# Kernel optimization log

Hardware: AMD Instinct MI355X
Metric: run time of the kernel (lower is better)

## Reference

```python
import jax, jax.numpy as jnp
import numpy as np

B, N, D = 2, 2048, 1024
H, ENC = 16, 8
HD = D // H
EPS = 1e-5


def _apply_rope(x, cos, sin):
    # x: [B,N,H,HD], cos/sin: [N,HD//2]
    c = cos[None, :, None, :]
    s = sin[None, :, None, :]
    x_re = x[..., 0::2]
    x_im = x[..., 1::2]
    out = jnp.stack([x_re * c - x_im * s, x_re * s + x_im * c], axis=-1)
    return out.reshape(x.shape)


def _rmsnorm(x):
    return x * jax.lax.rsqrt(jnp.mean(x * x, axis=-1, keepdims=True) + EPS)


def setup_inputs() -> dict:
    key = jax.random.key(0)
    ks = jax.random.split(key, 8)
    pos = jnp.arange(N, dtype=jnp.float32)[:, None]
    inv_freq = 1.0 / (10000.0 ** (jnp.arange(0, HD, 2, dtype=jnp.float32) / HD))  # [HD//2]
    ang = pos * inv_freq[None, :]
    std = 0.02
    return {
        "x": jax.random.normal(ks[0], (B, N, D), dtype=jnp.float32),
        "rope_cos": jnp.cos(ang),
        "rope_sin": jnp.sin(ang),
        "Wq": std * jax.random.normal(ks[1], (D, D), dtype=jnp.float32),
        "Wk": std * jax.random.normal(ks[2], (D, D), dtype=jnp.float32),
        "Wv": std * jax.random.normal(ks[3], (D, D), dtype=jnp.float32),
        "Wo_enc": std * jax.random.normal(ks[4], (H * HD, D), dtype=jnp.float32),
        "Wo_dec": std * jax.random.normal(ks[5], ((H - ENC) * HD, D), dtype=jnp.float32),
        "heads": H,
        "encoder_heads": ENC,
    }


def reference(x, rope_cos, rope_sin, Wq, Wk, Wv, Wo_enc, Wo_dec, heads, encoder_heads):
    b, n, d = x.shape
    hd = d // heads
    scale = hd ** (-0.5)
    q = (x @ Wq).reshape(b, n, heads, hd)
    k = (x @ Wk).reshape(b, n, heads, hd)
    v = (x @ Wv).reshape(b, n, heads, hd)
    q = _rmsnorm(_apply_rope(q, rope_cos, rope_sin))
    k = _rmsnorm(_apply_rope(k, rope_cos, rope_sin))
    # scores: [B,H,N,N]
    scores = jnp.einsum("bihd,bjhd->bhij", q, k) * scale
    causal = jnp.tril(jnp.ones((n, n), dtype=bool))  # [N,N]
    is_enc = (jnp.arange(heads) < encoder_heads)[:, None, None]  # [H,1,1]
    allow = jnp.logical_or(is_enc, causal[None, :, :])  # [H,N,N]
    scores = jnp.where(allow[None], scores, -jnp.inf)
    att = jax.nn.softmax(scores, axis=-1)
    out = jnp.einsum("bhij,bjhd->bihd", att, v)  # [B,N,H,HD]
    enc_out = out.reshape(b, n, heads * hd) @ Wo_enc
    dec_out = out[:, :, encoder_heads:, :].reshape(b, n, (heads - encoder_heads) * hd) @ Wo_dec
    return (enc_out, dec_out)
```

## Files before the change

### kernel.cpp

```cpp
#include <hip/hip_runtime.h>
#include <hip/hip_bf16.h>
#include <math.h>

#define B_    2
#define N_    2048
#define D_    1024
#define H_    16
#define ENC_  8
#define HD_   64
#define EPS_  1e-5f
#define M_    (B_ * N_)

typedef __bf16 bf16x8 __attribute__((ext_vector_type(8)));
typedef __bf16 bf16x2 __attribute__((ext_vector_type(2)));
typedef float  f32x4  __attribute__((ext_vector_type(4)));

#define MB(x) ((size_t)(x) * 1024 * 1024)

#define KSC_  0.18033688011112042f

#if __has_builtin(__builtin_amdgcn_exp2f)
#define EXP2F(x) __builtin_amdgcn_exp2f(x)
#else
#define EXP2F(x) exp2f(x)
#endif

__device__ __forceinline__ void gld16(const __bf16* g, __bf16* l) {
    __builtin_amdgcn_global_load_lds(
        (const __attribute__((address_space(1))) void*)g,
        (__attribute__((address_space(3))) void*)l,
        16, 0, 0);
}

template <typename OutT>
__device__ __forceinline__ void gemm_core(
    const __bf16* __restrict__ A, const __bf16* __restrict__ Bt,
    OutT* __restrict__ C, int K, int lda, int aoff, int ldc,
    int bm, int bn, __bf16* As, __bf16* Bs)
{
    const int tid  = threadIdx.x;
    const int w    = tid >> 6;
    const int lane = tid & 63;
    const int lrow = lane & 15;
    const int quad = lane >> 4;
    const int wr   = w >> 1;
    const int wc   = w & 1;

    const int sr = lane >> 2;
    const int sc = (lane & 3) * 8;
    const __bf16* Ag0 = A  + (size_t)(bm +      w * 16 + sr) * lda + aoff + sc;
    const __bf16* Ag1 = A  + (size_t)(bm + 64 + w * 16 + sr) * lda + aoff + sc;
    const __bf16* Bg0 = Bt + (size_t)(bn +      w * 16 + sr) * K + sc;
    const __bf16* Bg1 = Bt + (size_t)(bn + 64 + w * 16 + sr) * K + sc;
    __bf16* Al0 = &As[w * 512];
    __bf16* Al1 = &As[2048 + w * 512];
    __bf16* Bl0 = &Bs[w * 512];
    __bf16* Bl1 = &Bs[2048 + w * 512];

    f32x4 acc[4][4];
    #pragma unroll
    for (int i = 0; i < 4; ++i)
        #pragma unroll
        for (int j = 0; j < 4; ++j) acc[i][j] = (f32x4){0.f, 0.f, 0.f, 0.f};

    for (int k0 = 0; k0 < K; k0 += 32) {
        gld16(Ag0 + k0, Al0);
        gld16(Ag1 + k0, Al1);
        gld16(Bg0 + k0, Bl0);
        gld16(Bg1 + k0, Bl1);
        __syncthreads();

        bf16x8 af[4], bf[4];
        #pragma unroll
        for (int rt = 0; rt < 4; ++rt)
            af[rt] = *(const bf16x8*)&As[(wr * 64 + rt * 16 + lrow) * 32 + quad * 8];
        #pragma unroll
        for (int ct = 0; ct < 4; ++ct)
            bf[ct] = *(const bf16x8*)&Bs[(wc * 64 + ct * 16 + lrow) * 32 + quad * 8];

        #pragma unroll
        for (int rt = 0; rt < 4; ++rt)
            #pragma unroll
            for (int ct = 0; ct < 4; ++ct)
                acc[rt][ct] = __builtin_amdgcn_mfma_f32_16x16x32_bf16(
                    af[rt], bf[ct], acc[rt][ct], 0, 0, 0);
        __syncthreads();
    }

    #pragma unroll
    for (int rt = 0; rt < 4; ++rt)
        #pragma unroll
        for (int ct = 0; ct < 4; ++ct)
            #pragma unroll
            for (int r = 0; r < 4; ++r) {
                const int row = bm + wr * 64 + rt * 16 + quad * 4 + r;
                const int col = bn + wc * 64 + ct * 16 + lrow;
                C[(size_t)row * ldc + col] = (OutT)acc[rt][ct][r];
            }
}

__global__ __launch_bounds__(256) void gemm_qkv(
    const __bf16* __restrict__ A, const __bf16* __restrict__ Bt,
    __bf16* __restrict__ C)
{
    __shared__ __bf16 As[128 * 32];
    __shared__ __bf16 Bs[128 * 32];
    gemm_core<__bf16>(A, Bt, C, D_, D_, 0, 3072,
                      blockIdx.y * 128, blockIdx.x * 128, As, Bs);
}

__global__ __launch_bounds__(256) void gemm_out(
    const __bf16* __restrict__ A, const __bf16* __restrict__ Woe,
    const __bf16* __restrict__ Wod, float* __restrict__ Cenc,
    float* __restrict__ Cdec)
{
    __shared__ __bf16 As[128 * 32];
    __shared__ __bf16 Bs[128 * 32];
    const int bx = blockIdx.x;
    if (bx < 8) {
        gemm_core<float>(A, Woe, Cenc, 1024, D_, 0, D_,
                         blockIdx.y * 128, bx * 128, As, Bs);
    } else {
        gemm_core<float>(A, Wod, Cdec, 512, D_, 512, D_,
                         blockIdx.y * 128, (bx - 8) * 128, As, Bs);
    }
}

__global__ __launch_bounds__(256) void f32_to_bf16(
    const float* __restrict__ src, __bf16* __restrict__ dst)
{
    const size_t i = ((size_t)blockIdx.x * 256 + threadIdx.x) * 8;
    float4 a = *(const float4*)&src[i];
    float4 b = *(const float4*)&src[i + 4];
    bf16x8 o = {(__bf16)a.x, (__bf16)a.y, (__bf16)a.z, (__bf16)a.w,
                (__bf16)b.x, (__bf16)b.y, (__bf16)b.z, (__bf16)b.w};
    *(bf16x8*)&dst[i] = o;
}

struct WtArgs {
    const float* W[5];
    __bf16*      Wt[5];
    int          K[5];
    int          nyb[5];
};

__global__ __launch_bounds__(256) void wt_conv_all(WtArgs a)
{
    const int z = blockIdx.z;
    if (blockIdx.y >= a.nyb[z]) return;
    const float* W  = a.W[z];
    __bf16*      Wt = a.Wt[z];
    const int    K  = a.K[z];

    __shared__ __bf16 t[64][72];
    const int kb = blockIdx.y * 64;
    const int nb = blockIdx.x * 64;
    {
        const int kl = threadIdx.x >> 2;
        const int c0 = (threadIdx.x & 3) * 16;
        const float* src = W + (size_t)(kb + kl) * D_ + nb + c0;
        #pragma unroll
        for (int u = 0; u < 4; ++u) {
            float4 f = *(const float4*)&src[u * 4];
            t[c0 + u * 4 + 0][kl] = (__bf16)f.x;
            t[c0 + u * 4 + 1][kl] = (__bf16)f.y;
            t[c0 + u * 4 + 2][kl] = (__bf16)f.z;
            t[c0 + u * 4 + 3][kl] = (__bf16)f.w;
        }
    }
    __syncthreads();
    {
        const int nl  = threadIdx.x >> 2;
        const int k0c = (threadIdx.x & 3) * 16;
        __bf16* dst = Wt + (size_t)(nb + nl) * K + kb + k0c;
        *(bf16x8*)&dst[0] = *(const bf16x8*)&t[nl][k0c];
        *(bf16x8*)&dst[8] = *(const bf16x8*)&t[nl][k0c + 8];
    }
}

__global__ __launch_bounds__(256) void rope_vconv(
    const __bf16* __restrict__ qkv,
    const float* __restrict__ cs, const float* __restrict__ sn,
    __bf16* __restrict__ qbf, __bf16* __restrict__ kbf,
    __bf16* __restrict__ vt)
{
    if (blockIdx.x < 16384) {
        const int row  = blockIdx.x * 4 + (threadIdx.x >> 6);
        const int lane = threadIdx.x & 63;
        const int n    = (row >> 4) & (N_ - 1);
        const int b    = row >> 15;
        const int h    = row & 15;
        const int p    = lane >> 1;

        const float c = cs[n * (HD_ / 2) + p];
        const float s = sn[n * (HD_ / 2) + p];
        const size_t ibase = (size_t)(b * N_ + n) * 3072 + h * HD_ + lane;
        const size_t obase = ((size_t)(b * H_ + h) * N_ + n) * HD_ + lane;
        const bool odd = (lane & 1);

        {
            float val = (float)qkv[ibase];
            float partner = __shfl_xor(val, 1, 64);
            float r = odd ? fmaf(partner, s, val * c)
                          : (val * c - partner * s);
            float ss = r * r;
            #pragma unroll
            for (int off = 1; off < 64; off <<= 1) ss += __shfl_xor(ss, off, 64);
            qbf[obase] = (__bf16)(r * rsqrtf(ss * (1.0f / 64.0f) + EPS_) * KSC_);
        }
        {
            float val = (float)qkv[ibase + 1024];
            float partner = __shfl_xor(val, 1, 64);
            float r = odd ? fmaf(partner, s, val * c)
                          : (val * c - partner * s);
            float ss = r * r;
            #pragma unroll
            for (int off = 1; off < 64; off <<= 1) ss += __shfl_xor(ss, off, 64);
            kbf[obase] = (__bf16)(r * rsqrtf(ss * (1.0f / 64.0f) + EPS_));
        }
    } else {
        __shared__ __bf16 tile[64][72];
        const int bx = blockIdx.x - 16384;
        const int bh = bx >> 5;
        const int b  = bh >> 4, h = bh & 15;
        const int n0 = (bx & 31) * 64;
        {
            const int nl = threadIdx.x >> 2;
            const int d0 = (threadIdx.x & 3) * 16;
            const __bf16* src =
                qkv + (size_t)(b * N_ + n0 + nl) * 3072 + 2048 + h * HD_ + d0;
            bf16x8 v0 = *(const bf16x8*)&src[0];
            bf16x8 v1 = *(const bf16x8*)&src[8];
            #pragma unroll
            for (int e = 0; e < 8; ++e) {
                tile[d0 + e][nl]     = v0[e];
                tile[d0 + 8 + e][nl] = v1[e];
            }
        }
        __syncthreads();
        {
            const int dl = threadIdx.x >> 2;
            const int nc = (threadIdx.x & 3) * 16;
            __bf16* dst = vt + ((size_t)(bh * HD_ + dl)) * N_ + n0 + nc;
            bf16x8 o0, o1;
            #pragma unroll
            for (int e = 0; e < 8; ++e) {
                const int p0 = nc + e;
                const int p1 = nc + 8 + e;
                o0[e] = tile[dl][(p0 & ~31) + (((p0 >> 2) & 1) << 4)
                                 + (((p0 >> 3) & 3) << 2) + (p0 & 3)];
                o1[e] = tile[dl][(p1 & ~31) + (((p1 >> 2) & 1) << 4)
                                 + (((p1 >> 3) & 3) << 2) + (p1 & 3)];
            }
            *(bf16x8*)&dst[0] = o0;
            *(bf16x8*)&dst[8] = o1;
        }
    }
}

template <int NG, bool DEC>
__device__ __forceinline__ void attn_core(
    const __bf16* __restrict__ qbase, const __bf16* __restrict__ kbase,
    const __bf16* __restrict__ vbase, __bf16* __restrict__ o,
    int b, int h, int qb, int ntiles,
    __bf16 (*Ks)[4096], __bf16 (*Vs)[4096])
{
    const int tid  = threadIdx.x;
    const int w    = tid >> 6;
    const int lane = tid & 63;
    const int lrow = lane & 15;
    const int quad = lane >> 4;

    const __bf16* kg0 = kbase + (size_t)lane * HD_ + w * 8;
    const __bf16* kg1 = kbase + (size_t)lane * HD_ + (w + 4) * 8;
    const __bf16* vg  = vbase + (size_t)lane * N_;

    int i0g[NG];
    #pragma unroll
    for (int g = 0; g < NG; ++g) i0g[g] = qb * (NG * 64) + g * 64 + w * 16;

    bf16x8 qf[NG][2];
    #pragma unroll
    for (int g = 0; g < NG; ++g)
        #pragma unroll
        for (int kc = 0; kc < 2; ++kc)
            qf[g][kc] = *(const bf16x8*)
                &qbase[(size_t)(i0g[g] + lrow) * HD_ + kc * 32 + quad * 8];

    const f32x4 zero = {0.f, 0.f, 0.f, 0.f};
    f32x4 oacc[NG][4];
    float lsum[NG];
    #pragma unroll
    for (int g = 0; g < NG; ++g) {
        lsum[g] = 0.f;
        #pragma unroll
        for (int c = 0; c < 4; ++c) oacc[g][c] = zero;
    }

    auto stage = [&](int t, int bb) {
        const int j0 = t << 6;
        gld16(kg0 + (size_t)j0 * HD_, &Ks[bb][(w)     * 512]);
        gld16(kg1 + (size_t)j0 * HD_, &Ks[bb][(w + 4) * 512]);
        gld16(vg + j0 + w * 8,        &Vs[bb][(w)     * 512]);
        gld16(vg + j0 + (w + 4) * 8,  &Vs[bb][(w + 4) * 512]);
    };

    stage(0, 0);
    for (int t = 0; t < ntiles; ++t) {
        const int bb = t & 1;
        __syncthreads();
        if (t + 1 < ntiles) stage(t + 1, bb ^ 1);

        #pragma unroll
        for (int s = 0; s < 2; ++s) {
            const int jp = (t << 6) + s * 32;

            bf16x8 kf0 = *(const bf16x8*)&Ks[bb][((quad)     * 64 + s * 32 + lrow) * 8];
            bf16x8 kf1 = *(const bf16x8*)&Ks[bb][((4 + quad) * 64 + s * 32 + lrow) * 8];
            bf16x8 kf2 = *(const bf16x8*)&Ks[bb][((quad)     * 64 + s * 32 + 16 + lrow) * 8];
            bf16x8 kf3 = *(const bf16x8*)&Ks[bb][((4 + quad) * 64 + s * 32 + 16 + lrow) * 8];

            f32x4 s0[NG], s1[NG];
            #pragma unroll
            for (int g = 0; g < NG; ++g) { s0[g] = zero; s1[g] = zero; }
            #pragma unroll
            for (int g = 0; g < NG; ++g)
                s0[g] = __builtin_amdgcn_mfma_f32_16x16x32_bf16(kf0, qf[g][0], s0[g], 0, 0, 0);
            #pragma unroll
            for (int g = 0; g < NG; ++g)
                s0[g] = __builtin_amdgcn_mfma_f32_16x16x32_bf16(kf1, qf[g][1], s0[g], 0, 0, 0);
            #pragma unroll
            for (int g = 0; g < NG; ++g)
                s1[g] = __builtin_amdgcn_mfma_f32_16x16x32_bf16(kf2, qf[g][0], s1[g], 0, 0, 0);
            #pragma unroll
            for (int g = 0; g < NG; ++g)
                s1[g] = __builtin_amdgcn_mfma_f32_16x16x32_bf16(kf3, qf[g][1], s1[g], 0, 0, 0);

            bf16x8 pf[NG];
            #pragma unroll
            for (int g = 0; g < NG; ++g) {
                float pA[4], pB[4];
                if (DEC && (jp + 31 > i0g[g])) {
                    const int i = i0g[g] + lrow;
                    #pragma unroll
                    for (int r = 0; r < 4; ++r) {
                        const int k0 = jp + quad * 4 + r;
                        pA[r] = (k0      <= i) ? EXP2F(s0[g][r]) : 0.f;
                        pB[r] = (k0 + 16 <= i) ? EXP2F(s1[g][r]) : 0.f;
                    }
                } else {
                    #pragma unroll
                    for (int r = 0; r < 4; ++r) {
                        pA[r] = EXP2F(s0[g][r]);
                        pB[r] = EXP2F(s1[g][r]);
                    }
                }
                lsum[g] += (pA[0] + pA[1]) + (pA[2] + pA[3])
                         + (pB[0] + pB[1]) + (pB[2] + pB[3]);
                pf[g] = (bf16x8){(__bf16)pA[0], (__bf16)pA[1],
                                 (__bf16)pA[2], (__bf16)pA[3],
                                 (__bf16)pB[0], (__bf16)pB[1],
                                 (__bf16)pB[2], (__bf16)pB[3]};
            }

            bf16x8 vf0 = *(const bf16x8*)&Vs[bb][((s * 4 + quad) * 64 +  0 + lrow) * 8];
            bf16x8 vf1 = *(const bf16x8*)&Vs[bb][((s * 4 + quad) * 64 + 16 + lrow) * 8];
            bf16x8 vf2 = *(const bf16x8*)&Vs[bb][((s * 4 + quad) * 64 + 32 + lrow) * 8];
            bf16x8 vf3 = *(const bf16x8*)&Vs[bb][((s * 4 + quad) * 64 + 48 + lrow) * 8];

            #pragma unroll
            for (int g = 0; g < NG; ++g) {
                oacc[g][0] = __builtin_amdgcn_mfma_f32_16x16x32_bf16(pf[g], vf0, oacc[g][0], 0, 0, 0);
                oacc[g][1] = __builtin_amdgcn_mfma_f32_16x16x32_bf16(pf[g], vf1, oacc[g][1], 0, 0, 0);
                oacc[g][2] = __builtin_amdgcn_mfma_f32_16x16x32_bf16(pf[g], vf2, oacc[g][2], 0, 0, 0);
                oacc[g][3] = __builtin_amdgcn_mfma_f32_16x16x32_bf16(pf[g], vf3, oacc[g][3], 0, 0, 0);
            }
        }
    }

    float lrec[NG][4];
    #pragma unroll
    for (int g = 0; g < NG; ++g) {
        float s = lsum[g];
        s += __shfl_xor(s, 16, 64);
        s += __shfl_xor(s, 32, 64);
        s = 1.0f / s;
        #pragma unroll
        for (int r = 0; r < 4; ++r)
            lrec[g][r] = __shfl(s, quad * 4 + r, 64);
    }

    #pragma unroll
    for (int g = 0; g < NG; ++g)
        #pragma unroll
        for (int c = 0; c < 4; ++c)
            #pragma unroll
            for (int r = 0; r < 4; ++r) {
                const int i = i0g[g] + quad * 4 + r;
                o[(size_t)(b * N_ + i) * D_ + h * HD_ + c * 16 + lrow] =
                    (__bf16)(oacc[g][c][r] * lrec[g][r]);
            }
}

__global__ __launch_bounds__(256) void attn_mfma(
    const __bf16* __restrict__ qbf, const __bf16* __restrict__ kbf,
    const __bf16* __restrict__ vtbf, __bf16* __restrict__ o)
{
    __shared__ __bf16 Ks[2][4096];
    __shared__ __bf16 Vs[2][4096];

    if (blockIdx.x < 256) {
        const int e  = blockIdx.x & 15;
        const int bh = (e >> 3) * 16 + (e & 7);
        const int qb = blockIdx.x >> 4;
        attn_core<2, false>(
            qbf  + (size_t)bh * N_ * HD_, kbf + (size_t)bh * N_ * HD_,
            vtbf + (size_t)bh * HD_ * N_, o,
            bh >> 4, bh & 15, qb, N_ >> 6, Ks, Vs);
    } else {
        const int idx = blockIdx.x - 256;
        const int d   = idx & 15;
        const int bh  = (d >> 3) * 16 + 8 + (d & 7);
        const int qb  = 31 - (idx >> 4);
        attn_core<1, true>(
            qbf  + (size_t)bh * N_ * HD_, kbf + (size_t)bh * N_ * HD_,
            vtbf + (size_t)bh * HD_ * N_, o,
            bh >> 4, bh & 15, qb, qb + 1, Ks, Vs);
    }
}

extern "C" void kernel_launch(void* const* d_in, const int* in_sizes, int n_in,
                              void* d_out, int out_size, void* d_ws, size_t ws_size,
                              hipStream_t stream)
{
    const float* x   = (const float*)d_in[0];
    const float* cs  = (const float*)d_in[1];
    const float* sn  = (const float*)d_in[2];
    const float* Wq  = (const float*)d_in[3];
    const float* Wk  = (const float*)d_in[4];
    const float* Wv  = (const float*)d_in[5];
    const float* Woe = (const float*)d_in[6];
    const float* Wod = (const float*)d_in[7];

    float* enc_out = (float*)d_out;
    float* dec_out = enc_out + (size_t)M_ * D_;

    char* ws = (char*)d_ws;
    __bf16* xbf    = (__bf16*)(ws);
    __bf16* wqkv_t = (__bf16*)(ws + MB(8));
    __bf16* woe_t  = (__bf16*)(ws + MB(14));
    __bf16* wod_t  = (__bf16*)(ws + MB(16));
    __bf16* qkv    = (__bf16*)(ws + MB(17));
    __bf16* qbf    = (__bf16*)(ws + MB(41));
    __bf16* kbf    = (__bf16*)(ws + MB(49));
    __bf16* vtbf   = xbf;
    __bf16* obuf   = qkv;

    f32_to_bf16<<<(M_ * D_) / (256 * 8), 256, 0, stream>>>(x, xbf);

    WtArgs wa;
    wa.W[0] = Wq;  wa.Wt[0] = wqkv_t;                 wa.K[0] = 1024; wa.nyb[0] = 16;
    wa.W[1] = Wk;  wa.Wt[1] = wqkv_t + 1024 * 1024;   wa.K[1] = 1024; wa.nyb[1] = 16;
    wa.W[2] = Wv;  wa.Wt[2] = wqkv_t + 2048 * 1024;   wa.K[2] = 1024; wa.nyb[2] = 16;
    wa.W[3] = Woe; wa.Wt[3] = woe_t;                  wa.K[3] = 1024; wa.nyb[3] = 16;
    wa.W[4] = Wod; wa.Wt[4] = wod_t;                  wa.K[4] = 512;  wa.nyb[4] = 8;
    wt_conv_all<<<dim3(16, 16, 5), 256, 0, stream>>>(wa);

    gemm_qkv<<<dim3(3072 / 128, M_ / 128), 256, 0, stream>>>(xbf, wqkv_t, qkv);

    rope_vconv<<<16384 + 1024, 256, 0, stream>>>(qkv, cs, sn, qbf, kbf, vtbf);

    attn_mfma<<<dim3(768), 256, 0, stream>>>(qbf, kbf, vtbf, obuf);

    gemm_out<<<dim3(16, M_ / 128), 256, 0, stream>>>(
        obuf, woe_t, wod_t, enc_out, dec_out);
}
```

Before: 222.7 us.

## Fuse x conversion into weight conversion, add MFMA priority, reorder decoder blocks

Folds the x f32-to-bf16 conversion into the weight-conversion launch as eight extra z-slices, which removes one kernel launch. The attention MFMA sections are wrapped in s_setprio to raise wave priority while matrix ops issue. The decoder-head query-block order changes so the second half of the blocks runs the short causal blocks in ascending order, which alters load balance across the grid. These are three separate tweaks, each with small expected impact.

```diff
diff --git a/kernel.cpp b/kernel.cpp
--- a/kernel.cpp
+++ b/kernel.cpp
@@ -126,31 +126,32 @@
     }
 }
 
-__global__ __launch_bounds__(256) void f32_to_bf16(
-    const float* __restrict__ src, __bf16* __restrict__ dst)
-{
-    const size_t i = ((size_t)blockIdx.x * 256 + threadIdx.x) * 8;
-    float4 a = *(const float4*)&src[i];
-    float4 b = *(const float4*)&src[i + 4];
-    bf16x8 o = {(__bf16)a.x, (__bf16)a.y, (__bf16)a.z, (__bf16)a.w,
-                (__bf16)b.x, (__bf16)b.y, (__bf16)b.z, (__bf16)b.w};
-    *(bf16x8*)&dst[i] = o;
-}
-
 struct WtArgs {
     const float* W[5];
     __bf16*      Wt[5];
     int          K[5];
     int          nyb[5];
+    const float* x;
+    __bf16*      xbf;
 };
 
-__global__ __launch_bounds__(256) void wt_conv_all(WtArgs a)
+__global__ __launch_bounds__(256) void wt_conv_all(WtArgs ar)
 {
     const int z = blockIdx.z;
-    if (blockIdx.y >= a.nyb[z]) return;
-    const float* W  = a.W[z];
-    __bf16*      Wt = a.Wt[z];
-    const int    K  = a.K[z];
+    if (z >= 5) {
+        const int linear = (z - 5) * 256 + blockIdx.y * 16 + blockIdx.x;
+        const size_t i = ((size_t)linear * 256 + threadIdx.x) * 8;
+        float4 a = *(const float4*)&ar.x[i];
+        float4 b = *(const float4*)&ar.x[i + 4];
+        bf16x8 o = {(__bf16)a.x, (__bf16)a.y, (__bf16)a.z, (__bf16)a.w,
+                    (__bf16)b.x, (__bf16)b.y, (__bf16)b.z, (__bf16)b.w};
+        *(bf16x8*)&ar.xbf[i] = o;
+        return;
+    }
+    if (blockIdx.y >= ar.nyb[z]) return;
+    const float* W  = ar.W[z];
+    __bf16*      Wt = ar.Wt[z];
+    const int    K  = ar.K[z];
 
     __shared__ __bf16 t[64][72];
     const int kb = blockIdx.y * 64;
@@ -323,6 +324,7 @@
             f32x4 s0[NG], s1[NG];
             #pragma unroll
             for (int g = 0; g < NG; ++g) { s0[g] = zero; s1[g] = zero; }
+            __builtin_amdgcn_s_setprio(1);
             #pragma unroll
             for (int g = 0; g < NG; ++g)
                 s0[g] = __builtin_amdgcn_mfma_f32_16x16x32_bf16(kf0, qf[g][0], s0[g], 0, 0, 0);
@@ -335,6 +337,7 @@
             #pragma unroll
             for (int g = 0; g < NG; ++g)
                 s1[g] = __builtin_amdgcn_mfma_f32_16x16x32_bf16(kf3, qf[g][1], s1[g], 0, 0, 0);
+            __builtin_amdgcn_s_setprio(0);
 
             bf16x8 pf[NG];
             #pragma unroll
@@ -368,6 +371,7 @@
             bf16x8 vf2 = *(const bf16x8*)&Vs[bb][((s * 4 + quad) * 64 + 32 + lrow) * 8];
             bf16x8 vf3 = *(const bf16x8*)&Vs[bb][((s * 4 + quad) * 64 + 48 + lrow) * 8];
 
+            __builtin_amdgcn_s_setprio(1);
             #pragma unroll
             for (int g = 0; g < NG; ++g) {
                 oacc[g][0] = __builtin_amdgcn_mfma_f32_16x16x32_bf16(pf[g], vf0, oacc[g][0], 0, 0, 0);
@@ -375,6 +379,7 @@
                 oacc[g][2] = __builtin_amdgcn_mfma_f32_16x16x32_bf16(pf[g], vf2, oacc[g][2], 0, 0, 0);
                 oacc[g][3] = __builtin_amdgcn_mfma_f32_16x16x32_bf16(pf[g], vf3, oacc[g][3], 0, 0, 0);
             }
+            __builtin_amdgcn_s_setprio(0);
         }
     }
 
@@ -421,7 +426,8 @@
         const int idx = blockIdx.x - 256;
         const int d   = idx & 15;
         const int bh  = (d >> 3) * 16 + 8 + (d & 7);
-        const int qb  = 31 - (idx >> 4);
+        const int p   = idx >> 4;
+        const int qb  = (p < 16) ? (31 - p) : (p - 16);
         attn_core<1, true>(
             qbf  + (size_t)bh * N_ * HD_, kbf + (size_t)bh * N_ * HD_,
             vtbf + (size_t)bh * HD_ * N_, o,
@@ -456,15 +462,14 @@
     __bf16* vtbf   = xbf;
     __bf16* obuf   = qkv;
 
-    f32_to_bf16<<<(M_ * D_) / (256 * 8), 256, 0, stream>>>(x, xbf);
-
     WtArgs wa;
     wa.W[0] = Wq;  wa.Wt[0] = wqkv_t;                 wa.K[0] = 1024; wa.nyb[0] = 16;
     wa.W[1] = Wk;  wa.Wt[1] = wqkv_t + 1024 * 1024;   wa.K[1] = 1024; wa.nyb[1] = 16;
     wa.W[2] = Wv;  wa.Wt[2] = wqkv_t + 2048 * 1024;   wa.K[2] = 1024; wa.nyb[2] = 16;
     wa.W[3] = Woe; wa.Wt[3] = woe_t;                  wa.K[3] = 1024; wa.nyb[3] = 16;
     wa.W[4] = Wod; wa.Wt[4] = wod_t;                  wa.K[4] = 512;  wa.nyb[4] = 8;
-    wt_conv_all<<<dim3(16, 16, 5), 256, 0, stream>>>(wa);
+    wa.x = x; wa.xbf = xbf;
+    wt_conv_all<<<dim3(16, 16, 13), 256, 0, stream>>>(wa);
 
     gemm_qkv<<<dim3(3072 / 128, M_ / 128), 256, 0, stream>>>(xbf, wqkv_t, qkv);
 
```

Result: slower. 235.4 us (+5.7%).
